# Kernel tuning notes

Hardware: AMD Instinct MI355X
Metric: run time of the kernel (lower is better)

## Reference

```python
import jax, jax.numpy as jnp
import numpy as np

NUM_Q, DIM_S, SIZE_M = 10000, 128, 50
B, L = 64, 200


def setup_inputs() -> dict:
    key = jax.random.key(0)
    ks = jax.random.split(key, 16)
    return {
        "q": jax.random.randint(ks[0], (B, L), 0, NUM_Q),
        "r": jax.random.randint(ks[1], (B, L), 0, 2),
        "k_emb": jax.random.normal(ks[2], (NUM_Q, DIM_S), jnp.float32),
        "v_emb": jax.random.normal(ks[3], (2 * NUM_Q, DIM_S), jnp.float32),
        "Mk": jax.random.normal(ks[4], (SIZE_M, DIM_S), jnp.float32),
        "Mv0": jax.random.normal(ks[5], (SIZE_M, DIM_S), jnp.float32),
        "f_W": jax.random.normal(ks[6], (DIM_S, 2 * DIM_S), jnp.float32) * 0.05,
        "f_b": jax.random.normal(ks[7], (DIM_S,), jnp.float32) * 0.05,
        "p_W": jax.random.normal(ks[8], (1, DIM_S), jnp.float32) * 0.05,
        "p_b": jax.random.normal(ks[9], (1,), jnp.float32) * 0.05,
        "e_W": jax.random.normal(ks[10], (DIM_S, DIM_S), jnp.float32) * 0.05,
        "e_b": jax.random.normal(ks[11], (DIM_S,), jnp.float32) * 0.05,
        "a_W": jax.random.normal(ks[12], (DIM_S, DIM_S), jnp.float32) * 0.05,
        "a_b": jax.random.normal(ks[13], (DIM_S,), jnp.float32) * 0.05,
    }


def reference(q, r, k_emb, v_emb, Mk, Mv0, f_W, f_b, p_W, p_b, e_W, e_b, a_W, a_b):
    num_q = k_emb.shape[0]
    x = q + num_q * r                      # [B, L] indices into v_emb
    Bsz = q.shape[0]
    k = k_emb[q]                           # [B, L, D]
    v = v_emb[x]                           # [B, L, D]
    w = jax.nn.softmax(jnp.einsum('bld,md->blm', k, Mk), axis=-1)  # [B, L, M]
    e = jax.nn.sigmoid(v @ e_W.T + e_b)    # [B, L, D]
    a = jnp.tanh(v @ a_W.T + a_b)          # [B, L, D]

    Mv_init = jnp.broadcast_to(Mv0, (Bsz,) + Mv0.shape)  # [B, M, D]

    def step(Mvt, inp):
        et, at, wt = inp  # [B, D], [B, D], [B, M]
        Mvt = Mvt * (1.0 - wt[:, :, None] * et[:, None, :]) + wt[:, :, None] * at[:, None, :]
        return Mvt, Mvt

    _, Mv_states = jax.lax.scan(
        step, Mv_init,
        (e.transpose(1, 0, 2), a.transpose(1, 0, 2), w.transpose(1, 0, 2)))
    # Mv: [B, L+1, M, D] (state before each update, plus final)
    Mv = jnp.concatenate([Mv_init[None], Mv_states], axis=0).transpose(1, 0, 2, 3)
    read = jnp.einsum('blm,blmd->bld', w, Mv[:, :-1])   # [B, L, D]
    f = jnp.tanh(jnp.concatenate([read, k], axis=-1) @ f_W.T + f_b)
    p = jax.nn.sigmoid(f @ p_W.T + p_b)[..., 0]          # [B, L]
    return p, Mv
```

## Files before the change

### kernel.cpp

```cpp
#include <hip/hip_runtime.h>
#include <math.h>

#define BB 64
#define LL 200
#define DD 128
#define MM 50
#define NQ 10000
#define NPOS (BB * LL)
#define LC 20
#define NC 10

__global__ __launch_bounds__(256) void k_wea(
    const int* __restrict__ q, const int* __restrict__ r,
    const float* __restrict__ k_emb, const float* __restrict__ v_emb,
    const float* __restrict__ Mk,
    const float* __restrict__ e_W, const float* __restrict__ e_b,
    const float* __restrict__ a_W, const float* __restrict__ a_b,
    float* __restrict__ w_ws, float* __restrict__ e_ws, float* __restrict__ a_ws)
{
    __shared__ float k_lds[16][DD];
    __shared__ float v_lds[16][DD];
    __shared__ float lg[16][MM];

    const int tid = threadIdx.x;
    const int p0  = blockIdx.x * 16;

    #pragma unroll
    for (int rep = 0; rep < 2; ++rep) {
        int idx = rep * 256 + tid;
        int pos = idx >> 5;
        int c4  = idx & 31;
        int gp  = p0 + pos;
        int qi  = q[gp];
        int xi  = qi + NQ * r[gp];
        float4 kv = *(const float4*)(k_emb + (size_t)qi * DD + c4 * 4);
        float4 vv = *(const float4*)(v_emb + (size_t)xi * DD + c4 * 4);
        *(float4*)(&k_lds[pos][c4 * 4]) = kv;
        *(float4*)(&v_lds[pos][c4 * 4]) = vv;
    }
    __syncthreads();

    for (int j = tid; j < 16 * MM; j += 256) {
        int pos = j / MM;
        int m   = j - pos * MM;
        const float* mk = Mk + m * DD;
        float acc = 0.f;
        #pragma unroll 4
        for (int jj = 0; jj < DD; ++jj)
            acc = fmaf(k_lds[pos][jj], mk[jj], acc);
        lg[pos][m] = acc;
    }
    __syncthreads();

    if (tid < 16) {
        int pos = tid;
        float mx = -INFINITY;
        for (int m = 0; m < MM; ++m) mx = fmaxf(mx, lg[pos][m]);
        float s = 0.f;
        for (int m = 0; m < MM; ++m) {
            float e_ = expf(lg[pos][m] - mx);
            lg[pos][m] = e_;
            s += e_;
        }
        float inv = 1.f / s;
        float* wout = w_ws + (size_t)(p0 + pos) * MM;
        for (int m = 0; m < MM; ++m) wout[m] = lg[pos][m] * inv;
    }

    const int i    = tid & 127;
    const int half = tid >> 7;
    float acc_e[8], acc_a[8];
    const float eb = e_b[i];
    const float ab = a_b[i];
    #pragma unroll
    for (int p = 0; p < 8; ++p) { acc_e[p] = eb; acc_a[p] = ab; }

    const float4* ew = (const float4*)(e_W + (size_t)i * DD);
    const float4* aw = (const float4*)(a_W + (size_t)i * DD);
    #pragma unroll 4
    for (int j4 = 0; j4 < 32; ++j4) {
        float4 we = ew[j4];
        float4 wa = aw[j4];
        #pragma unroll
        for (int p = 0; p < 8; ++p) {
            const float* vp = &v_lds[half * 8 + p][j4 * 4];
            acc_e[p] = fmaf(we.x, vp[0], acc_e[p]);
            acc_e[p] = fmaf(we.y, vp[1], acc_e[p]);
            acc_e[p] = fmaf(we.z, vp[2], acc_e[p]);
            acc_e[p] = fmaf(we.w, vp[3], acc_e[p]);
            acc_a[p] = fmaf(wa.x, vp[0], acc_a[p]);
            acc_a[p] = fmaf(wa.y, vp[1], acc_a[p]);
            acc_a[p] = fmaf(wa.z, vp[2], acc_a[p]);
            acc_a[p] = fmaf(wa.w, vp[3], acc_a[p]);
        }
    }
    #pragma unroll
    for (int p = 0; p < 8; ++p) {
        int gp = p0 + half * 8 + p;
        e_ws[(size_t)gp * DD + i] = 1.f / (1.f + expf(-acc_e[p]));
        a_ws[(size_t)gp * DD + i] = tanhf(acc_a[p]);
    }
}

__global__ __launch_bounds__(512) void k_scanA(
    const float* __restrict__ w_ws, const float* __restrict__ e_ws,
    const float* __restrict__ a_ws,
    float* __restrict__ A_ws, float* __restrict__ B_ws)
{
    __shared__ float w_lds[LC * MM];

    const int b   = blockIdx.x / NC;
    const int c   = blockIdx.x % NC;
    const int tid = threadIdx.x;
    const int d   = tid & 127;
    const int g   = tid >> 7;
    int moff = g * 13; if (g == 3) moff = 38;
    const int mcnt = (g < 2) ? 13 : 12;

    const float* wsrc = w_ws + ((size_t)b * LL + c * LC) * MM;
    for (int idx = tid; idx < LC * MM; idx += 512) w_lds[idx] = wsrc[idx];
    __syncthreads();

    float A[13], Bv[13];
    #pragma unroll
    for (int mi = 0; mi < 13; ++mi) { A[mi] = 1.f; Bv[mi] = 0.f; }

    for (int ll = 0; ll < LC; ++ll) {
        const int gp = b * LL + c * LC + ll;
        const float e = e_ws[(size_t)gp * DD + d];
        const float a = a_ws[(size_t)gp * DD + d];
        const float* wl = w_lds + ll * MM + moff;
        #pragma unroll
        for (int mi = 0; mi < 13; ++mi) {
            if (mi < mcnt) {
                float w_ = wl[mi];
                float cc = fmaf(-w_, e, 1.f);
                A[mi] *= cc;
                Bv[mi] = fmaf(Bv[mi], cc, w_ * a);
            }
        }
    }

    float* Ao = A_ws + ((size_t)b * NC + c) * MM * DD + (size_t)moff * DD + d;
    float* Bo = B_ws + ((size_t)b * NC + c) * MM * DD + (size_t)moff * DD + d;
    #pragma unroll
    for (int mi = 0; mi < 13; ++mi) {
        if (mi < mcnt) { Ao[mi * DD] = A[mi]; Bo[mi * DD] = Bv[mi]; }
    }
}

__global__ __launch_bounds__(256) void k_scanB(
    const float* __restrict__ Mv0,
    float* __restrict__ A_ws,
    const float* __restrict__ B_ws)
{
    const int g  = blockIdx.x * 256 + threadIdx.x;
    const int d  = g & (DD - 1);
    const int md = g >> 7;
    const int m  = md % MM;
    const int b  = md / MM;

    float S = Mv0[m * DD + d];
    const size_t base = ((size_t)b * NC * MM + m) * DD + d;
    #pragma unroll
    for (int c = 0; c < NC; ++c) {
        const size_t off = base + (size_t)c * MM * DD;
        const float Ac = A_ws[off];
        const float Bc = B_ws[off];
        A_ws[off] = S;
        S = fmaf(Ac, S, Bc);
    }
}

__global__ __launch_bounds__(512) void k_scanC(
    const float* __restrict__ Sentry,
    const float* __restrict__ w_ws, const float* __restrict__ e_ws,
    const float* __restrict__ a_ws,
    float* __restrict__ read_ws, float* __restrict__ out_Mv)
{
    __shared__ float w_lds[LC * MM];
    __shared__ float red[2][4][DD];

    const int b   = blockIdx.x / NC;
    const int c   = blockIdx.x % NC;
    const int tid = threadIdx.x;
    const int d   = tid & 127;
    const int g   = tid >> 7;
    int moff = g * 13; if (g == 3) moff = 38;
    const int mcnt = (g < 2) ? 13 : 12;

    const float* wsrc = w_ws + ((size_t)b * LL + c * LC) * MM;
    for (int idx = tid; idx < LC * MM; idx += 512) w_lds[idx] = wsrc[idx];

    float S[13];
    const float* Sp = Sentry + ((size_t)b * NC + c) * MM * DD + (size_t)moff * DD + d;
    #pragma unroll
    for (int mi = 0; mi < 13; ++mi)
        if (mi < mcnt) S[mi] = Sp[mi * DD];

    float* outb = out_Mv + (size_t)b * (LL + 1) * MM * DD;
    if (c == 0) {
        #pragma unroll
        for (int mi = 0; mi < 13; ++mi)
            if (mi < mcnt) outb[(moff + mi) * DD + d] = S[mi];
    }
    __syncthreads();

    for (int ll = 0; ll < LC; ++ll) {
        const int l  = c * LC + ll;
        const int gp = b * LL + l;
        const float e = e_ws[(size_t)gp * DD + d];
        const float a = a_ws[(size_t)gp * DD + d];
        const float* wl = w_lds + ll * MM + moff;

        float racc = 0.f;
        float* o = outb + (size_t)(l + 1) * MM * DD + d;
        #pragma unroll
        for (int mi = 0; mi < 13; ++mi) {
            if (mi < mcnt) {
                float w_ = wl[mi];
                racc = fmaf(w_, S[mi], racc);
                S[mi] = fmaf(w_, fmaf(-S[mi], e, a), S[mi]);
                o[(moff + mi) * DD] = S[mi];
            }
        }
        red[ll & 1][g][d] = racc;
        __syncthreads();
        if (g == 0)
            read_ws[(size_t)gp * DD + d] =
                red[ll & 1][0][d] + red[ll & 1][1][d] +
                red[ll & 1][2][d] + red[ll & 1][3][d];
    }
}

__global__ __launch_bounds__(128) void k_fp(
    const int* __restrict__ q,
    const float* __restrict__ k_emb,
    const float* __restrict__ read_ws,
    const float* __restrict__ f_W, const float* __restrict__ f_b,
    const float* __restrict__ p_W, const float* __restrict__ p_b,
    float* __restrict__ out_p)
{
    __shared__ float cat[16][2 * DD];
    __shared__ float fv[16][DD];

    const int tid = threadIdx.x;
    const int p0  = blockIdx.x * 16;

    #pragma unroll
    for (int rep = 0; rep < 8; ++rep) {
        int idx = rep * 128 + tid;
        int pos = idx >> 6;
        int c4  = idx & 63;
        int gp  = p0 + pos;
        float4 val;
        if (c4 < 32) val = *(const float4*)(read_ws + (size_t)gp * DD + c4 * 4);
        else         val = *(const float4*)(k_emb + (size_t)q[gp] * DD + (c4 - 32) * 4);
        *(float4*)(&cat[pos][c4 * 4]) = val;
    }
    __syncthreads();

    const int i = tid;
    float acc[16];
    const float fb = f_b[i];
    #pragma unroll
    for (int p = 0; p < 16; ++p) acc[p] = fb;

    const float4* fw = (const float4*)(f_W + (size_t)i * (2 * DD));
    #pragma unroll 2
    for (int j4 = 0; j4 < 64; ++j4) {
        float4 wv = fw[j4];
        #pragma unroll
        for (int p = 0; p < 16; ++p) {
            const float* cp = &cat[p][j4 * 4];
            acc[p] = fmaf(wv.x, cp[0], acc[p]);
            acc[p] = fmaf(wv.y, cp[1], acc[p]);
            acc[p] = fmaf(wv.z, cp[2], acc[p]);
            acc[p] = fmaf(wv.w, cp[3], acc[p]);
        }
    }
    #pragma unroll
    for (int p = 0; p < 16; ++p) fv[p][i] = tanhf(acc[p]);
    __syncthreads();

    const int pos = tid >> 3;
    const int l8  = tid & 7;
    float partial = 0.f;
    #pragma unroll
    for (int ii = l8; ii < DD; ii += 8)
        partial = fmaf(fv[pos][ii], p_W[ii], partial);
    partial += __shfl_down(partial, 4, 64);
    partial += __shfl_down(partial, 2, 64);
    partial += __shfl_down(partial, 1, 64);
    if (l8 == 0)
        out_p[p0 + pos] = 1.f / (1.f + expf(-(partial + p_b[0])));
}

extern "C" void kernel_launch(void* const* d_in, const int* in_sizes, int n_in,
                              void* d_out, int out_size, void* d_ws, size_t ws_size,
                              hipStream_t stream)
{
    const int*   q     = (const int*)d_in[0];
    const int*   r     = (const int*)d_in[1];
    const float* k_emb = (const float*)d_in[2];
    const float* v_emb = (const float*)d_in[3];
    const float* Mk    = (const float*)d_in[4];
    const float* Mv0   = (const float*)d_in[5];
    const float* f_W   = (const float*)d_in[6];
    const float* f_b   = (const float*)d_in[7];
    const float* p_W   = (const float*)d_in[8];
    const float* p_b   = (const float*)d_in[9];
    const float* e_W   = (const float*)d_in[10];
    const float* e_b   = (const float*)d_in[11];
    const float* a_W   = (const float*)d_in[12];
    const float* a_b   = (const float*)d_in[13];

    float* out_p  = (float*)d_out;
    float* out_Mv = out_p + NPOS;

    float* w_ws    = (float*)d_ws;
    float* e_ws    = w_ws + (size_t)NPOS * MM;
    float* a_ws    = e_ws + (size_t)NPOS * DD;
    float* read_ws = a_ws + (size_t)NPOS * DD;
    float* A_ws    = read_ws + (size_t)NPOS * DD;
    float* B_ws    = A_ws + (size_t)BB * NC * MM * DD;

    hipLaunchKernelGGL(k_wea, dim3(NPOS / 16), dim3(256), 0, stream,
                       q, r, k_emb, v_emb, Mk, e_W, e_b, a_W, a_b,
                       w_ws, e_ws, a_ws);
    hipLaunchKernelGGL(k_scanA, dim3(BB * NC), dim3(512), 0, stream,
                       w_ws, e_ws, a_ws, A_ws, B_ws);
    hipLaunchKernelGGL(k_scanB, dim3((BB * MM * DD) / 256), dim3(256), 0, stream,
                       Mv0, A_ws, B_ws);
    hipLaunchKernelGGL(k_scanC, dim3(BB * NC), dim3(512), 0, stream,
                       A_ws, w_ws, e_ws, a_ws, read_ws, out_Mv);
    hipLaunchKernelGGL(k_fp, dim3(NPOS / 16), dim3(128), 0, stream,
                       q, k_emb, read_ws, f_W, f_b, p_W, p_b, out_p);
}
```

Baseline: 222.7 us.

## Split softmax and e/a projections into separate kernels with 64-position tiles

Splits the fused w/e/a kernel into k_w (key-memory softmax) and k_ea (erase/add projections). Both k_ea and the output kernel k_fp now tile 64 positions per block, with one position per lane. Weight rows are read as wave-uniform float4 loads while each lane keeps many output accumulators in registers. The aim is to reuse each weight load across 64 positions instead of 16, and to replace the serial per-position dot loop for the Mk logits. The cost is one extra kernel launch and much higher register pressure (64 accumulators in k_ea), which may lower occupancy.

```diff
diff --git a/kernel.cpp b/kernel.cpp
--- a/kernel.cpp
+++ b/kernel.cpp
@@ -10,95 +10,125 @@
 #define LC 20
 #define NC 10
 
-__global__ __launch_bounds__(256) void k_wea(
+__device__ __forceinline__ float dot4(float4 a, float4 b, float c) {
+    return fmaf(a.x, b.x, fmaf(a.y, b.y, fmaf(a.z, b.z, fmaf(a.w, b.w, c))));
+}
+
+__global__ __launch_bounds__(256) void k_w(
+    const int* __restrict__ q, const float* __restrict__ k_emb,
+    const float* __restrict__ Mk, float* __restrict__ w_ws)
+{
+    __shared__ float k_lds[64][132];
+    __shared__ float lg[64][52];
+    __shared__ float winv[64];
+
+    const int tid = threadIdx.x;
+    const int p0  = blockIdx.x * 64;
+
+    #pragma unroll
+    for (int rep = 0; rep < 8; ++rep) {
+        int idx = rep * 256 + tid;
+        int pos = idx >> 5, c4 = idx & 31;
+        int qi  = q[p0 + pos];
+        *(float4*)&k_lds[pos][c4 * 4] =
+            *(const float4*)(k_emb + (size_t)qi * DD + c4 * 4);
+    }
+    __syncthreads();
+
+    const int w    = __builtin_amdgcn_readfirstlane(tid >> 6);
+    const int pos  = tid & 63;
+    const int m0   = w * 13;
+    const int mcnt = (w == 3) ? 11 : 13;
+
+    float acc[13];
+    #pragma unroll
+    for (int s = 0; s < 13; ++s) acc[s] = 0.f;
+
+    for (int j4 = 0; j4 < 32; ++j4) {
+        float4 k4 = *(float4*)&k_lds[pos][j4 * 4];
+        #pragma unroll
+        for (int s = 0; s < 13; ++s)
+            if (s < mcnt)
+                acc[s] = dot4(k4, *(const float4*)(Mk + (size_t)(m0 + s) * DD + j4 * 4), acc[s]);
+    }
+    #pragma unroll
+    for (int s = 0; s < 13; ++s)
+        if (s < mcnt) lg[pos][m0 + s] = acc[s];
+    __syncthreads();
+
+    if (tid < 64) {
+        float mx = -INFINITY;
+        for (int m = 0; m < MM; ++m) mx = fmaxf(mx, lg[tid][m]);
+        float sum = 0.f;
+        for (int m = 0; m < MM; ++m) {
+            float e = expf(lg[tid][m] - mx);
+            lg[tid][m] = e;
+            sum += e;
+        }
+        winv[tid] = 1.f / sum;
+    }
+    __syncthreads();
+
+    for (int idx = tid; idx < 64 * MM; idx += 256) {
+        int pp = idx / MM, m = idx - pp * MM;
+        w_ws[(size_t)(p0 + pp) * MM + m] = lg[pp][m] * winv[pp];
+    }
+}
+
+__global__ __launch_bounds__(128) void k_ea(
     const int* __restrict__ q, const int* __restrict__ r,
-    const float* __restrict__ k_emb, const float* __restrict__ v_emb,
-    const float* __restrict__ Mk,
+    const float* __restrict__ v_emb,
     const float* __restrict__ e_W, const float* __restrict__ e_b,
     const float* __restrict__ a_W, const float* __restrict__ a_b,
-    float* __restrict__ w_ws, float* __restrict__ e_ws, float* __restrict__ a_ws)
-{
-    __shared__ float k_lds[16][DD];
-    __shared__ float v_lds[16][DD];
-    __shared__ float lg[16][MM];
-
-    const int tid = threadIdx.x;
-    const int p0  = blockIdx.x * 16;
-
-    #pragma unroll
-    for (int rep = 0; rep < 2; ++rep) {
-        int idx = rep * 256 + tid;
-        int pos = idx >> 5;
-        int c4  = idx & 31;
+    float* __restrict__ e_ws, float* __restrict__ a_ws)
+{
+    __shared__ float v_lds[64][132];
+    __shared__ float buf_e[2][64][36];
+    __shared__ float buf_a[2][64][36];
+
+    const int tid = threadIdx.x;
+    const int pg  = blockIdx.x >> 1, h = blockIdx.x & 1;
+    const int p0  = pg * 64;
+
+    #pragma unroll
+    for (int rep = 0; rep < 16; ++rep) {
+        int idx = rep * 128 + tid;
+        int pos = idx >> 5, c4 = idx & 31;
         int gp  = p0 + pos;
-        int qi  = q[gp];
-        int xi  = qi + NQ * r[gp];
-        float4 kv = *(const float4*)(k_emb + (size_t)qi * DD + c4 * 4);
-        float4 vv = *(const float4*)(v_emb + (size_t)xi * DD + c4 * 4);
-        *(float4*)(&k_lds[pos][c4 * 4]) = kv;
-        *(float4*)(&v_lds[pos][c4 * 4]) = vv;
-    }
-    __syncthreads();
-
-    for (int j = tid; j < 16 * MM; j += 256) {
-        int pos = j / MM;
-        int m   = j - pos * MM;
-        const float* mk = Mk + m * DD;
-        float acc = 0.f;
-        #pragma unroll 4
-        for (int jj = 0; jj < DD; ++jj)
-            acc = fmaf(k_lds[pos][jj], mk[jj], acc);
-        lg[pos][m] = acc;
-    }
-    __syncthreads();
-
-    if (tid < 16) {
-        int pos = tid;
-        float mx = -INFINITY;
-        for (int m = 0; m < MM; ++m) mx = fmaxf(mx, lg[pos][m]);
-        float s = 0.f;
-        for (int m = 0; m < MM; ++m) {
-            float e_ = expf(lg[pos][m] - mx);
-            lg[pos][m] = e_;
-            s += e_;
+        int xi  = q[gp] + NQ * r[gp];
+        *(float4*)&v_lds[pos][c4 * 4] =
+            *(const float4*)(v_emb + (size_t)xi * DD + c4 * 4);
+    }
+    __syncthreads();
+
+    const int w    = __builtin_amdgcn_readfirstlane(tid >> 6);
+    const int lane = tid & 63;
+    const int i0   = h * 64 + w * 32;
+
+    float ae[32], aa[32];
+    #pragma unroll
+    for (int ii = 0; ii < 32; ++ii) { ae[ii] = e_b[i0 + ii]; aa[ii] = a_b[i0 + ii]; }
+
+    for (int j4 = 0; j4 < 32; ++j4) {
+        float4 v4 = *(float4*)&v_lds[lane][j4 * 4];
+        #pragma unroll
+        for (int ii = 0; ii < 32; ++ii) {
+            ae[ii] = dot4(v4, *(const float4*)(e_W + (size_t)(i0 + ii) * DD + j4 * 4), ae[ii]);
+            aa[ii] = dot4(v4, *(const float4*)(a_W + (size_t)(i0 + ii) * DD + j4 * 4), aa[ii]);
         }
-        float inv = 1.f / s;
-        float* wout = w_ws + (size_t)(p0 + pos) * MM;
-        for (int m = 0; m < MM; ++m) wout[m] = lg[pos][m] * inv;
-    }
-
-    const int i    = tid & 127;
-    const int half = tid >> 7;
-    float acc_e[8], acc_a[8];
-    const float eb = e_b[i];
-    const float ab = a_b[i];
-    #pragma unroll
-    for (int p = 0; p < 8; ++p) { acc_e[p] = eb; acc_a[p] = ab; }
-
-    const float4* ew = (const float4*)(e_W + (size_t)i * DD);
-    const float4* aw = (const float4*)(a_W + (size_t)i * DD);
-    #pragma unroll 4
-    for (int j4 = 0; j4 < 32; ++j4) {
-        float4 we = ew[j4];
-        float4 wa = aw[j4];
-        #pragma unroll
-        for (int p = 0; p < 8; ++p) {
-            const float* vp = &v_lds[half * 8 + p][j4 * 4];
-            acc_e[p] = fmaf(we.x, vp[0], acc_e[p]);
-            acc_e[p] = fmaf(we.y, vp[1], acc_e[p]);
-            acc_e[p] = fmaf(we.z, vp[2], acc_e[p]);
-            acc_e[p] = fmaf(we.w, vp[3], acc_e[p]);
-            acc_a[p] = fmaf(wa.x, vp[0], acc_a[p]);
-            acc_a[p] = fmaf(wa.y, vp[1], acc_a[p]);
-            acc_a[p] = fmaf(wa.z, vp[2], acc_a[p]);
-            acc_a[p] = fmaf(wa.w, vp[3], acc_a[p]);
-        }
-    }
-    #pragma unroll
-    for (int p = 0; p < 8; ++p) {
-        int gp = p0 + half * 8 + p;
-        e_ws[(size_t)gp * DD + i] = 1.f / (1.f + expf(-acc_e[p]));
-        a_ws[(size_t)gp * DD + i] = tanhf(acc_a[p]);
+    }
+
+    #pragma unroll
+    for (int ii = 0; ii < 32; ++ii) {
+        buf_e[w][lane][ii] = 1.f / (1.f + expf(-ae[ii]));
+        buf_a[w][lane][ii] = tanhf(aa[ii]);
+    }
+    #pragma unroll
+    for (int rep = 0; rep < 8; ++rep) {
+        int idx = rep * 64 + lane;
+        int pp = idx >> 3, c4 = idx & 7;
+        *(float4*)(e_ws + (size_t)(p0 + pp) * DD + i0 + c4 * 4) = *(float4*)&buf_e[w][pp][c4 * 4];
+        *(float4*)(a_ws + (size_t)(p0 + pp) * DD + i0 + c4 * 4) = *(float4*)&buf_a[w][pp][c4 * 4];
     }
 }
 
@@ -233,7 +263,7 @@
     }
 }
 
-__global__ __launch_bounds__(128) void k_fp(
+__global__ __launch_bounds__(256) void k_fp(
     const int* __restrict__ q,
     const float* __restrict__ k_emb,
     const float* __restrict__ read_ws,
@@ -241,59 +271,58 @@
     const float* __restrict__ p_W, const float* __restrict__ p_b,
     float* __restrict__ out_p)
 {
-    __shared__ float cat[16][2 * DD];
-    __shared__ float fv[16][DD];
-
-    const int tid = threadIdx.x;
-    const int p0  = blockIdx.x * 16;
+    __shared__ float rd_l[64][132];
+    __shared__ float kk_l[64][132];
+    __shared__ float p_red[4][64];
+
+    const int tid = threadIdx.x;
+    const int p0  = blockIdx.x * 64;
 
     #pragma unroll
     for (int rep = 0; rep < 8; ++rep) {
-        int idx = rep * 128 + tid;
-        int pos = idx >> 6;
-        int c4  = idx & 63;
+        int idx = rep * 256 + tid;
+        int pos = idx >> 5, c4 = idx & 31;
         int gp  = p0 + pos;
-        float4 val;
-        if (c4 < 32) val = *(const float4*)(read_ws + (size_t)gp * DD + c4 * 4);
-        else         val = *(const float4*)(k_emb + (size_t)q[gp] * DD + (c4 - 32) * 4);
-        *(float4*)(&cat[pos][c4 * 4]) = val;
-    }
-    __syncthreads();
-
-    const int i = tid;
-    float acc[16];
-    const float fb = f_b[i];
-    #pragma unroll
-    for (int p = 0; p < 16; ++p) acc[p] = fb;
-
-    const float4* fw = (const float4*)(f_W + (size_t)i * (2 * DD));
-    #pragma unroll 2
-    for (int j4 = 0; j4 < 64; ++j4) {
-        float4 wv = fw[j4];
-        #pragma unroll
-        for (int p = 0; p < 16; ++p) {
-            const float* cp = &cat[p][j4 * 4];
-            acc[p] = fmaf(wv.x, cp[0], acc[p]);
-            acc[p] = fmaf(wv.y, cp[1], acc[p]);
-            acc[p] = fmaf(wv.z, cp[2], acc[p]);
-            acc[p] = fmaf(wv.w, cp[3], acc[p]);
-        }
-    }
-    #pragma unroll
-    for (int p = 0; p < 16; ++p) fv[p][i] = tanhf(acc[p]);
-    __syncthreads();
-
-    const int pos = tid >> 3;
-    const int l8  = tid & 7;
-    float partial = 0.f;
-    #pragma unroll
-    for (int ii = l8; ii < DD; ii += 8)
-        partial = fmaf(fv[pos][ii], p_W[ii], partial);
-    partial += __shfl_down(partial, 4, 64);
-    partial += __shfl_down(partial, 2, 64);
-    partial += __shfl_down(partial, 1, 64);
-    if (l8 == 0)
-        out_p[p0 + pos] = 1.f / (1.f + expf(-(partial + p_b[0])));
+        *(float4*)&rd_l[pos][c4 * 4] =
+            *(const float4*)(read_ws + (size_t)gp * DD + c4 * 4);
+        int qi = q[gp];
+        *(float4*)&kk_l[pos][c4 * 4] =
+            *(const float4*)(k_emb + (size_t)qi * DD + c4 * 4);
+    }
+    __syncthreads();
+
+    const int w    = __builtin_amdgcn_readfirstlane(tid >> 6);
+    const int lane = tid & 63;
+    const int i0   = w * 32;
+
+    float acc[32];
+    #pragma unroll
+    for (int ii = 0; ii < 32; ++ii) acc[ii] = f_b[i0 + ii];
+
+    for (int j4 = 0; j4 < 32; ++j4) {
+        float4 r4 = *(float4*)&rd_l[lane][j4 * 4];
+        #pragma unroll
+        for (int ii = 0; ii < 32; ++ii)
+            acc[ii] = dot4(r4, *(const float4*)(f_W + (size_t)(i0 + ii) * (2 * DD) + j4 * 4), acc[ii]);
+    }
+    for (int j4 = 0; j4 < 32; ++j4) {
+        float4 k4 = *(float4*)&kk_l[lane][j4 * 4];
+        #pragma unroll
+        for (int ii = 0; ii < 32; ++ii)
+            acc[ii] = dot4(k4, *(const float4*)(f_W + (size_t)(i0 + ii) * (2 * DD) + DD + j4 * 4), acc[ii]);
+    }
+
+    float pp = 0.f;
+    #pragma unroll
+    for (int ii = 0; ii < 32; ++ii)
+        pp = fmaf(tanhf(acc[ii]), p_W[i0 + ii], pp);
+    p_red[w][lane] = pp;
+    __syncthreads();
+
+    if (tid < 64) {
+        float s = p_red[0][tid] + p_red[1][tid] + p_red[2][tid] + p_red[3][tid] + p_b[0];
+        out_p[p0 + tid] = 1.f / (1.f + expf(-s));
+    }
 }
 
 extern "C" void kernel_launch(void* const* d_in, const int* in_sizes, int n_in,
@@ -325,15 +354,16 @@
     float* A_ws    = read_ws + (size_t)NPOS * DD;
     float* B_ws    = A_ws + (size_t)BB * NC * MM * DD;
 
-    hipLaunchKernelGGL(k_wea, dim3(NPOS / 16), dim3(256), 0, stream,
-                       q, r, k_emb, v_emb, Mk, e_W, e_b, a_W, a_b,
-                       w_ws, e_ws, a_ws);
+    hipLaunchKernelGGL(k_w, dim3(NPOS / 64), dim3(256), 0, stream,
+                       q, k_emb, Mk, w_ws);
+    hipLaunchKernelGGL(k_ea, dim3(2 * NPOS / 64), dim3(128), 0, stream,
+                       q, r, v_emb, e_W, e_b, a_W, a_b, e_ws, a_ws);
     hipLaunchKernelGGL(k_scanA, dim3(BB * NC), dim3(512), 0, stream,
                        w_ws, e_ws, a_ws, A_ws, B_ws);
     hipLaunchKernelGGL(k_scanB, dim3((BB * MM * DD) / 256), dim3(256), 0, stream,
                        Mv0, A_ws, B_ws);
     hipLaunchKernelGGL(k_scanC, dim3(BB * NC), dim3(512), 0, stream,
                        A_ws, w_ws, e_ws, a_ws, read_ws, out_Mv);
-    hipLaunchKernelGGL(k_fp, dim3(NPOS / 16), dim3(128), 0, stream,
+    hipLaunchKernelGGL(k_fp, dim3(NPOS / 64), dim3(256), 0, stream,
                        q, k_emb, read_ws, f_W, f_b, p_W, p_b, out_p);
 }
```

Result: slower. 339.1 us (+52.3%).

## Stage weight matrices in padded LDS tiles for embedding and output GEMVs

Applied to the files above, without the earlier changes.

The e/a projection and the f/p output kernels now stage 32-row chunks of the weight matrices into padded shared memory instead of each thread streaming its own weight row from global memory. Each thread computes two positions per chunk, with a shuffle reduction for the final p dot product. Mk is transposed into LDS to get conflict-free logits, and softmax normalisation writes are spread across all threads. In exchange there are more block barriers and more LDS traffic per block, and less register-level reuse across positions. The larger LDS footprint may also lower occupancy.

```diff
diff --git a/kernel.cpp b/kernel.cpp
--- a/kernel.cpp
+++ b/kernel.cpp
@@ -10,6 +10,15 @@
 #define LC 20
 #define NC 10
 
+#define PAD_KV 132
+#define MKT_LD 52
+#define EW_LD 133
+#define FW_LD 261
+
+__device__ __forceinline__ float dot4(float4 a, float4 b, float c) {
+    return fmaf(a.x, b.x, fmaf(a.y, b.y, fmaf(a.z, b.z, fmaf(a.w, b.w, c))));
+}
+
 __global__ __launch_bounds__(256) void k_wea(
     const int* __restrict__ q, const int* __restrict__ r,
     const float* __restrict__ k_emb, const float* __restrict__ v_emb,
@@ -18,9 +27,15 @@
     const float* __restrict__ a_W, const float* __restrict__ a_b,
     float* __restrict__ w_ws, float* __restrict__ e_ws, float* __restrict__ a_ws)
 {
-    __shared__ float k_lds[16][DD];
-    __shared__ float v_lds[16][DD];
-    __shared__ float lg[16][MM];
+    __shared__ float smem[2112 + 2 * 32 * EW_LD];
+    __shared__ float lg[16][MKT_LD];
+    __shared__ float winv16[16];
+
+    float* k_l  = smem;
+    float* mkT  = smem + 2112;
+    float* v_l  = smem;
+    float* ew_l = smem + 2112;
+    float* aw_l = smem + 2112 + 32 * EW_LD;
 
     const int tid = threadIdx.x;
     const int p0  = blockIdx.x * 16;
@@ -28,77 +43,85 @@
     #pragma unroll
     for (int rep = 0; rep < 2; ++rep) {
         int idx = rep * 256 + tid;
-        int pos = idx >> 5;
-        int c4  = idx & 31;
+        int pos = idx >> 5, c4 = idx & 31;
+        int qi  = q[p0 + pos];
+        *(float4*)&k_l[pos * PAD_KV + c4 * 4] =
+            *(const float4*)(k_emb + (size_t)qi * DD + c4 * 4);
+    }
+    for (int idx = tid; idx < MM * DD; idx += 256) {
+        int m = idx >> 7, jj = idx & 127;
+        mkT[jj * MKT_LD + m] = Mk[idx];
+    }
+    __syncthreads();
+
+    for (int j = tid; j < 16 * MM; j += 256) {
+        int pos = j / MM, m = j - pos * MM;
+        const float* kp = &k_l[pos * PAD_KV];
+        float acc = 0.f;
+        #pragma unroll 8
+        for (int jj = 0; jj < DD; ++jj)
+            acc = fmaf(kp[jj], mkT[jj * MKT_LD + m], acc);
+        lg[pos][m] = acc;
+    }
+    __syncthreads();
+
+    if (tid < 16) {
+        float mx = -INFINITY;
+        for (int m = 0; m < MM; ++m) mx = fmaxf(mx, lg[tid][m]);
+        float sum = 0.f;
+        for (int m = 0; m < MM; ++m) {
+            float e = expf(lg[tid][m] - mx);
+            lg[tid][m] = e;
+            sum += e;
+        }
+        winv16[tid] = 1.f / sum;
+    }
+    __syncthreads();
+
+    for (int idx = tid; idx < 16 * MM; idx += 256) {
+        int pos = idx / MM, m = idx - pos * MM;
+        w_ws[(size_t)(p0 + pos) * MM + m] = lg[pos][m] * winv16[pos];
+    }
+    #pragma unroll
+    for (int rep = 0; rep < 2; ++rep) {
+        int idx = rep * 256 + tid;
+        int pos = idx >> 5, c4 = idx & 31;
         int gp  = p0 + pos;
-        int qi  = q[gp];
-        int xi  = qi + NQ * r[gp];
-        float4 kv = *(const float4*)(k_emb + (size_t)qi * DD + c4 * 4);
-        float4 vv = *(const float4*)(v_emb + (size_t)xi * DD + c4 * 4);
-        *(float4*)(&k_lds[pos][c4 * 4]) = kv;
-        *(float4*)(&v_lds[pos][c4 * 4]) = vv;
-    }
-    __syncthreads();
-
-    for (int j = tid; j < 16 * MM; j += 256) {
-        int pos = j / MM;
-        int m   = j - pos * MM;
-        const float* mk = Mk + m * DD;
-        float acc = 0.f;
-        #pragma unroll 4
-        for (int jj = 0; jj < DD; ++jj)
-            acc = fmaf(k_lds[pos][jj], mk[jj], acc);
-        lg[pos][m] = acc;
-    }
-    __syncthreads();
-
-    if (tid < 16) {
-        int pos = tid;
-        float mx = -INFINITY;
-        for (int m = 0; m < MM; ++m) mx = fmaxf(mx, lg[pos][m]);
-        float s = 0.f;
-        for (int m = 0; m < MM; ++m) {
-            float e_ = expf(lg[pos][m] - mx);
-            lg[pos][m] = e_;
-            s += e_;
-        }
-        float inv = 1.f / s;
-        float* wout = w_ws + (size_t)(p0 + pos) * MM;
-        for (int m = 0; m < MM; ++m) wout[m] = lg[pos][m] * inv;
-    }
-
-    const int i    = tid & 127;
-    const int half = tid >> 7;
-    float acc_e[8], acc_a[8];
-    const float eb = e_b[i];
-    const float ab = a_b[i];
-    #pragma unroll
-    for (int p = 0; p < 8; ++p) { acc_e[p] = eb; acc_a[p] = ab; }
-
-    const float4* ew = (const float4*)(e_W + (size_t)i * DD);
-    const float4* aw = (const float4*)(a_W + (size_t)i * DD);
-    #pragma unroll 4
-    for (int j4 = 0; j4 < 32; ++j4) {
-        float4 we = ew[j4];
-        float4 wa = aw[j4];
-        #pragma unroll
-        for (int p = 0; p < 8; ++p) {
-            const float* vp = &v_lds[half * 8 + p][j4 * 4];
-            acc_e[p] = fmaf(we.x, vp[0], acc_e[p]);
-            acc_e[p] = fmaf(we.y, vp[1], acc_e[p]);
-            acc_e[p] = fmaf(we.z, vp[2], acc_e[p]);
-            acc_e[p] = fmaf(we.w, vp[3], acc_e[p]);
-            acc_a[p] = fmaf(wa.x, vp[0], acc_a[p]);
-            acc_a[p] = fmaf(wa.y, vp[1], acc_a[p]);
-            acc_a[p] = fmaf(wa.z, vp[2], acc_a[p]);
-            acc_a[p] = fmaf(wa.w, vp[3], acc_a[p]);
-        }
-    }
-    #pragma unroll
-    for (int p = 0; p < 8; ++p) {
-        int gp = p0 + half * 8 + p;
-        e_ws[(size_t)gp * DD + i] = 1.f / (1.f + expf(-acc_e[p]));
-        a_ws[(size_t)gp * DD + i] = tanhf(acc_a[p]);
+        int xi  = q[gp] + NQ * r[gp];
+        *(float4*)&v_l[pos * PAD_KV + c4 * 4] =
+            *(const float4*)(v_emb + (size_t)xi * DD + c4 * 4);
+    }
+
+    const int i = tid & 31;
+    const int g = tid >> 5;
+    const int pos0 = g * 2, pos1 = g * 2 + 1;
+
+    for (int c = 0; c < 4; ++c) {
+        __syncthreads();
+        for (int idx = tid; idx < 32 * 32; idx += 256) {
+            int row = idx >> 5, c4 = idx & 31;
+            *(float4*)&ew_l[row * EW_LD + c4 * 4] =
+                *(const float4*)(e_W + (size_t)(c * 32 + row) * DD + c4 * 4);
+            *(float4*)&aw_l[row * EW_LD + c4 * 4] =
+                *(const float4*)(a_W + (size_t)(c * 32 + row) * DD + c4 * 4);
+        }
+        __syncthreads();
+
+        float ae0 = 0.f, ae1 = 0.f, aa0 = 0.f, aa1 = 0.f;
+        for (int j4 = 0; j4 < 32; ++j4) {
+            float4 we = *(float4*)&ew_l[i * EW_LD + j4 * 4];
+            float4 wa = *(float4*)&aw_l[i * EW_LD + j4 * 4];
+            float4 v0 = *(float4*)&v_l[pos0 * PAD_KV + j4 * 4];
+            float4 v1 = *(float4*)&v_l[pos1 * PAD_KV + j4 * 4];
+            ae0 = dot4(v0, we, ae0);  ae1 = dot4(v1, we, ae1);
+            aa0 = dot4(v0, wa, aa0);  aa1 = dot4(v1, wa, aa1);
+        }
+        const int ig = c * 32 + i;
+        const float ebv = e_b[ig], abv = a_b[ig];
+        e_ws[(size_t)(p0 + pos0) * DD + ig] = 1.f / (1.f + expf(-(ae0 + ebv)));
+        e_ws[(size_t)(p0 + pos1) * DD + ig] = 1.f / (1.f + expf(-(ae1 + ebv)));
+        a_ws[(size_t)(p0 + pos0) * DD + ig] = tanhf(aa0 + abv);
+        a_ws[(size_t)(p0 + pos1) * DD + ig] = tanhf(aa1 + abv);
     }
 }
 
@@ -233,7 +256,7 @@
     }
 }
 
-__global__ __launch_bounds__(128) void k_fp(
+__global__ __launch_bounds__(256) void k_fp(
     const int* __restrict__ q,
     const float* __restrict__ k_emb,
     const float* __restrict__ read_ws,
@@ -241,59 +264,61 @@
     const float* __restrict__ p_W, const float* __restrict__ p_b,
     float* __restrict__ out_p)
 {
-    __shared__ float cat[16][2 * DD];
-    __shared__ float fv[16][DD];
+    __shared__ float cat_l[16][260];
+    __shared__ float fw_l[32 * FW_LD];
 
     const int tid = threadIdx.x;
     const int p0  = blockIdx.x * 16;
 
     #pragma unroll
-    for (int rep = 0; rep < 8; ++rep) {
-        int idx = rep * 128 + tid;
-        int pos = idx >> 6;
-        int c4  = idx & 63;
+    for (int rep = 0; rep < 4; ++rep) {
+        int idx = rep * 256 + tid;
+        int pos = idx >> 6, c4 = idx & 63;
         int gp  = p0 + pos;
         float4 val;
         if (c4 < 32) val = *(const float4*)(read_ws + (size_t)gp * DD + c4 * 4);
         else         val = *(const float4*)(k_emb + (size_t)q[gp] * DD + (c4 - 32) * 4);
-        *(float4*)(&cat[pos][c4 * 4]) = val;
-    }
-    __syncthreads();
-
-    const int i = tid;
-    float acc[16];
-    const float fb = f_b[i];
-    #pragma unroll
-    for (int p = 0; p < 16; ++p) acc[p] = fb;
-
-    const float4* fw = (const float4*)(f_W + (size_t)i * (2 * DD));
-    #pragma unroll 2
-    for (int j4 = 0; j4 < 64; ++j4) {
-        float4 wv = fw[j4];
-        #pragma unroll
-        for (int p = 0; p < 16; ++p) {
-            const float* cp = &cat[p][j4 * 4];
-            acc[p] = fmaf(wv.x, cp[0], acc[p]);
-            acc[p] = fmaf(wv.y, cp[1], acc[p]);
-            acc[p] = fmaf(wv.z, cp[2], acc[p]);
-            acc[p] = fmaf(wv.w, cp[3], acc[p]);
-        }
-    }
-    #pragma unroll
-    for (int p = 0; p < 16; ++p) fv[p][i] = tanhf(acc[p]);
-    __syncthreads();
-
-    const int pos = tid >> 3;
-    const int l8  = tid & 7;
-    float partial = 0.f;
-    #pragma unroll
-    for (int ii = l8; ii < DD; ii += 8)
-        partial = fmaf(fv[pos][ii], p_W[ii], partial);
-    partial += __shfl_down(partial, 4, 64);
-    partial += __shfl_down(partial, 2, 64);
-    partial += __shfl_down(partial, 1, 64);
-    if (l8 == 0)
-        out_p[p0 + pos] = 1.f / (1.f + expf(-(partial + p_b[0])));
+        *(float4*)&cat_l[pos][c4 * 4] = val;
+    }
+
+    const int i = tid & 31;
+    const int g = tid >> 5;
+    const int pos0 = g * 2, pos1 = g * 2 + 1;
+
+    float pp0 = 0.f, pp1 = 0.f;
+
+    for (int c = 0; c < 4; ++c) {
+        __syncthreads();
+        for (int idx = tid; idx < 32 * 64; idx += 256) {
+            int row = idx >> 6, c4 = idx & 63;
+            *(float4*)&fw_l[row * FW_LD + c4 * 4] =
+                *(const float4*)(f_W + (size_t)(c * 32 + row) * (2 * DD) + c4 * 4);
+        }
+        __syncthreads();
+
+        float a0 = 0.f, a1 = 0.f;
+        for (int j4 = 0; j4 < 64; ++j4) {
+            float4 fw4 = *(float4*)&fw_l[i * FW_LD + j4 * 4];
+            float4 c0  = *(float4*)&cat_l[pos0][j4 * 4];
+            float4 c1  = *(float4*)&cat_l[pos1][j4 * 4];
+            a0 = dot4(c0, fw4, a0);
+            a1 = dot4(c1, fw4, a1);
+        }
+        const int ig = c * 32 + i;
+        const float fb = f_b[ig], pw = p_W[ig];
+        pp0 = fmaf(tanhf(a0 + fb), pw, pp0);
+        pp1 = fmaf(tanhf(a1 + fb), pw, pp1);
+    }
+
+    #pragma unroll
+    for (int mask = 16; mask >= 1; mask >>= 1) {
+        pp0 += __shfl_xor(pp0, mask, 64);
+        pp1 += __shfl_xor(pp1, mask, 64);
+    }
+    if (i == 0) {
+        out_p[p0 + pos0] = 1.f / (1.f + expf(-(pp0 + p_b[0])));
+        out_p[p0 + pos1] = 1.f / (1.f + expf(-(pp1 + p_b[0])));
+    }
 }
 
 extern "C" void kernel_launch(void* const* d_in, const int* in_sizes, int n_in,
@@ -334,6 +359,6 @@
                        Mv0, A_ws, B_ws);
     hipLaunchKernelGGL(k_scanC, dim3(BB * NC), dim3(512), 0, stream,
                        A_ws, w_ws, e_ws, a_ws, read_ws, out_Mv);
-    hipLaunchKernelGGL(k_fp, dim3(NPOS / 16), dim3(128), 0, stream,
+    hipLaunchKernelGGL(k_fp, dim3(NPOS / 16), dim3(256), 0, stream,
                        q, k_emb, read_ws, f_W, f_b, p_W, p_b, out_p);
 }
```

After: 308.1 us. 38.3% more time.
